# Optimization experiments

Measured on AMD Instinct MI355X. Metric: run time of the kernel, lower is better.

Reference implementation:

```python
import jax, jax.numpy as jnp
import numpy as np

B, S, D, H, E, K = 2, 1024, 1024, 4096, 8, 2
HE = 4 * D  # expert FFN inner dim
LN_EPS = 1e-5


def layernorm(x, g, b):
    m = x.mean(-1, keepdims=True)
    v = ((x - m) ** 2).mean(-1, keepdims=True)
    return (x - m) * jax.lax.rsqrt(v + LN_EPS) * g + b


def pos_encoding(S, D):
    pos = jnp.arange(S, dtype=jnp.float32)[:, None]
    i = jnp.arange(0, D, 2, dtype=jnp.float32)
    div = jnp.exp(-(jnp.log(10000.0)) * i / D)
    pe = jnp.zeros((S, D), dtype=jnp.float32)
    pe = pe.at[:, 0::2].set(jnp.sin(pos * div))
    pe = pe.at[:, 1::2].set(jnp.cos(pos * div))
    return pe


def setup_inputs() -> dict:
    key = jax.random.key(0)
    ks = jax.random.split(key, 16)
    w = lambda k, sh, s=0.02: (jax.random.normal(k, sh, dtype=jnp.float32) * s)
    return {
        "x": jax.random.normal(ks[0], (B, S, D), dtype=jnp.float32),
        # router: LayerNorm -> Linear(D,H) -> GELU -> Linear(H,E)
        "r_ln_g": jnp.ones((D,), jnp.float32), "r_ln_b": jnp.zeros((D,), jnp.float32),
        "r_w1": w(ks[1], (D, H)), "r_b1": jnp.zeros((H,), jnp.float32),
        "r_w2": w(ks[2], (H, E)), "r_b2": jnp.zeros((E,), jnp.float32),
        "temperature": jnp.ones((1,), jnp.float32) * 0.07,
        # stacked expert params: LayerNorm -> Linear(D,HE) -> GELU -> Linear(HE,D)
        "e_ln_g": jnp.ones((E, D), jnp.float32), "e_ln_b": jnp.zeros((E, D), jnp.float32),
        "e_w1": w(ks[3], (E, D, HE)), "e_b1": jnp.zeros((E, HE), jnp.float32),
        "e_w2": w(ks[4], (E, HE, D)), "e_b2": jnp.zeros((E, D), jnp.float32),
        # combiner: LayerNorm -> Linear(D,2D) -> GELU -> Linear(2D,D)
        "c_ln_g": jnp.ones((D,), jnp.float32), "c_ln_b": jnp.zeros((D,), jnp.float32),
        "c_w1": w(ks[5], (D, 2 * D)), "c_b1": jnp.zeros((2 * D,), jnp.float32),
        "c_w2": w(ks[6], (2 * D, D)), "c_b2": jnp.zeros((D,), jnp.float32),
        "o_ln_g": jnp.ones((D,), jnp.float32), "o_ln_b": jnp.zeros((D,), jnp.float32),
    }


def reference(x, r_ln_g, r_ln_b, r_w1, r_b1, r_w2, r_b2, temperature,
              e_ln_g, e_ln_b, e_w1, e_b1, e_w2, e_b2,
              c_ln_g, c_ln_b, c_w1, c_b1, c_w2, c_b2, o_ln_g, o_ln_b):
    gelu = lambda t: jax.nn.gelu(t, approximate=False)
    h = x + pos_encoding(S, D)[None]  # [B,S,D]
    # router logits with learned temperature
    r = layernorm(h, r_ln_g, r_ln_b)
    r = gelu(jnp.einsum("bsd,dh->bsh", r, r_w1) + r_b1)
    logits = (jnp.einsum("bsh,he->bse", r, r_w2) + r_b2) / temperature
    probs = jax.nn.softmax(logits, axis=-1)  # [B,S,E]
    topk_p, topk_i = jax.lax.top_k(probs, K)
    # sparse gate [B,S,E]: softmax prob on selected experts, 0 elsewhere
    gate = (jax.nn.one_hot(topk_i, E, dtype=probs.dtype) * topk_p[..., None]).sum(-2)
    # per-expert FFN on all tokens (dense reference of dispatch/compute/combine)
    m = h.mean(-1, keepdims=True)
    v = ((h - m) ** 2).mean(-1, keepdims=True)
    xhat = (h - m) * jax.lax.rsqrt(v + LN_EPS)  # [B,S,D], shared LN stats
    y = xhat[None] * e_ln_g[:, None, None, :] + e_ln_b[:, None, None, :]  # [E,B,S,D]
    f = gelu(jnp.einsum("ebsd,edh->ebsh", y, e_w1) + e_b1[:, None, None, :])
    f = jnp.einsum("ebsh,ehd->ebsd", f, e_w2) + e_b2[:, None, None, :]
    combined = jnp.einsum("bse,ebsd->bsd", gate, f)
    # expert combiner MLP + residual + output norm
    c = layernorm(combined, c_ln_g, c_ln_b)
    c = gelu(jnp.einsum("bsd,de->bse", c, c_w1) + c_b1)
    c = jnp.einsum("bse,ed->bsd", c, c_w2) + c_b2
    return layernorm(h + c, o_ln_g, o_ln_b)
```

## Files before the change

### kernel.cpp

```cpp
#include <hip/hip_runtime.h>
#include <stdint.h>

#define TOK 2048
#define DD  1024
#define RH  4096
#define HE  4096
#define NE  8
#define CH  2048
#define MAXTILE 40
#define MAXROWS 5120
#define KSC2 2

using bf16x8 = __attribute__((ext_vector_type(8))) short;
using f32x4  = __attribute__((ext_vector_type(4))) float;

__device__ __forceinline__ unsigned short f2bf(float f) {
  union { float f; uint32_t u; } v; v.f = f;
  uint32_t r = (v.u + 0x7fffu + ((v.u >> 16) & 1u)) >> 16;
  return (unsigned short)r;
}
__device__ __forceinline__ float bf2f(unsigned short h) {
  union { uint32_t u; float f; } v; v.u = ((uint32_t)h) << 16;
  return v.f;
}
__device__ __forceinline__ float gelu_f(float x) {
  return 0.5f * x * (1.0f + erff(x * 0.70710678118654752440f));
}

#define GLD(SRC, DST) __builtin_amdgcn_global_load_lds( \
    (const __attribute__((address_space(1))) uint32_t*)(const void*)(SRC), \
    (__attribute__((address_space(3))) uint32_t*)(void*)(DST), 16, 0, 0)

__device__ __forceinline__ void block_ln_stats(float s1, float s2, float& mean, float& rstd) {
  #pragma unroll
  for (int off = 32; off > 0; off >>= 1) {
    s1 += __shfl_down(s1, off);
    s2 += __shfl_down(s2, off);
  }
  __shared__ float sh[8];
  int tid = threadIdx.x;
  if ((tid & 63) == 0) { sh[tid >> 6] = s1; sh[4 + (tid >> 6)] = s2; }
  __syncthreads();
  float t1 = sh[0] + sh[1] + sh[2] + sh[3];
  float t2 = sh[4] + sh[5] + sh[6] + sh[7];
  mean = t1 * (1.0f / 1024.0f);
  float var = t2 * (1.0f / 1024.0f) - mean * mean;
  rstd = rsqrtf(var + 1e-5f);
}

__global__ void k_prep(const float* __restrict__ x, float* __restrict__ h,
                       float* __restrict__ xh32, unsigned short* __restrict__ xhi,
                       unsigned short* __restrict__ xlo, int* __restrict__ cnt,
                       int* __restrict__ fillc, int* __restrict__ nflag,
                       int* __restrict__ tok_of) {
  int t = blockIdx.x;
  int s = t & 1023;
  int tid = threadIdx.x;
  float4 xv = ((const float4*)(x + (size_t)t * DD))[tid];
  float v[4]; float s1 = 0.f, s2 = 0.f;
  #pragma unroll
  for (int kp = 0; kp < 2; ++kp) {
    float i2 = (float)(tid * 4 + kp * 2);
    float div = expf(-9.2103403719761836f * i2 * (1.0f / 1024.0f));
    float ang = (float)s * div;
    float sn, cs;
    sincosf(ang, &sn, &cs);
    float xe = (kp == 0) ? xv.x : xv.z;
    float xo = (kp == 0) ? xv.y : xv.w;
    v[kp * 2] = xe + sn; v[kp * 2 + 1] = xo + cs;
  }
  #pragma unroll
  for (int k = 0; k < 4; ++k) { s1 += v[k]; s2 += v[k] * v[k]; }
  float mean, rstd;
  block_ln_stats(s1, s2, mean, rstd);
  float4 ho; ho.x = v[0]; ho.y = v[1]; ho.z = v[2]; ho.w = v[3];
  ((float4*)(h + (size_t)t * DD))[tid] = ho;
  float xn[4]; unsigned short hh[4], ll[4];
  #pragma unroll
  for (int k = 0; k < 4; ++k) {
    xn[k] = (v[k] - mean) * rstd;
    hh[k] = f2bf(xn[k]);
    ll[k] = f2bf(xn[k] - bf2f(hh[k]));
  }
  float4 xo4; xo4.x = xn[0]; xo4.y = xn[1]; xo4.z = xn[2]; xo4.w = xn[3];
  ((float4*)(xh32 + (size_t)t * DD))[tid] = xo4;
  ushort4 h4; h4.x = hh[0]; h4.y = hh[1]; h4.z = hh[2]; h4.w = hh[3];
  ((ushort4*)(xhi + (size_t)t * DD))[tid] = h4;
  ushort4 l4; l4.x = ll[0]; l4.y = ll[1]; l4.z = ll[2]; l4.w = ll[3];
  ((ushort4*)(xlo + (size_t)t * DD))[tid] = l4;
  if (t == 0) {
    for (int i = tid; i < MAXROWS; i += 256) tok_of[i] = 0;
    if (tid < NE) { cnt[tid] = 0; fillc[tid] = 0; }
    if (tid == 0) nflag[0] = 0;
  }
}

__global__ void k_tconv(const float* __restrict__ in, const float* __restrict__ g,
                        unsigned short* __restrict__ out, int D, int N,
                        long long in_bs, long long g_bs, long long out_bs) {
  __shared__ float tile[64][65];
  int e = blockIdx.z;
  const float* inb = in + (size_t)e * in_bs;
  unsigned short* outb = out + (size_t)e * out_bs;
  int n0 = blockIdx.x * 64, d0 = blockIdx.y * 64;
  int c4 = threadIdx.x & 15;
  int r0 = threadIdx.x >> 4;
  #pragma unroll
  for (int rr = 0; rr < 4; ++rr) {
    int dl = r0 + rr * 16;
    float4 v = *(const float4*)(inb + (size_t)(d0 + dl) * N + n0 + c4 * 4);
    if (g) {
      float gv = g[(size_t)e * g_bs + d0 + dl];
      v.x *= gv; v.y *= gv; v.z *= gv; v.w *= gv;
    }
    tile[dl][c4 * 4 + 0] = v.x; tile[dl][c4 * 4 + 1] = v.y;
    tile[dl][c4 * 4 + 2] = v.z; tile[dl][c4 * 4 + 3] = v.w;
  }
  __syncthreads();
  int q = threadIdx.x & 15;
  int nb = threadIdx.x >> 4;
  #pragma unroll
  for (int rr = 0; rr < 4; ++rr) {
    int nl = nb + rr * 16;
    ushort4 o;
    o.x = f2bf(tile[q * 4 + 0][nl]); o.y = f2bf(tile[q * 4 + 1][nl]);
    o.z = f2bf(tile[q * 4 + 2][nl]); o.w = f2bf(tile[q * 4 + 3][nl]);
    *(ushort4*)(outb + (size_t)(n0 + nl) * D + d0 + q * 4) = o;
  }
}

__global__ void k_tconv_split(const float* __restrict__ in, const float* __restrict__ g,
                              unsigned short* __restrict__ oh, unsigned short* __restrict__ ol,
                              float* __restrict__ o32, int D, int N) {
  __shared__ float tile[32][33];
  int n0 = blockIdx.x * 32, d0 = blockIdx.y * 32;
  int tn = threadIdx.x & 31, tr = threadIdx.x >> 5;
  #pragma unroll
  for (int rr = 0; rr < 4; ++rr) {
    int dl = tr + rr * 8;
    float v = in[(size_t)(d0 + dl) * N + n0 + tn];
    if (g) v *= g[d0 + dl];
    tile[dl][tn] = v;
  }
  __syncthreads();
  #pragma unroll
  for (int rr = 0; rr < 4; ++rr) {
    int nl = tr + rr * 8;
    float v = tile[tn][nl];
    size_t off = (size_t)(n0 + nl) * D + d0 + tn;
    unsigned short hi = f2bf(v);
    oh[off] = hi;
    ol[off] = f2bf(v - bf2f(hi));
    o32[off] = v;
  }
}

__global__ void k_foldbias(const float* __restrict__ w, const float* __restrict__ lnb,
                           const float* __restrict__ b1, float* __restrict__ outb,
                           int D, int N, long long w_bs, long long lnb_bs,
                           long long b_bs, long long o_bs) {
  int e = blockIdx.y;
  int n = blockIdx.x * 256 + threadIdx.x;
  const float* wb = w + (size_t)e * w_bs;
  const float* lb = lnb + (size_t)e * lnb_bs;
  float acc = b1[(size_t)e * b_bs + n];
  for (int d = 0; d < D; ++d) {
    float l = lb[d];
    if (l != 0.f) acc += l * wb[(size_t)d * N + n];
  }
  outb[(size_t)e * o_bs + n] = acc;
}

template <int DO_GELU, int OUT_BF16>
__global__ __launch_bounds__(256)
void k_gemm_n64(const unsigned short* __restrict__ A, const unsigned short* __restrict__ B,
                const float* __restrict__ bias, void* __restrict__ Cv, int N, int K,
                int kslice, long long c_slice) {
  __shared__ __align__(16) unsigned short As[128 * 32];
  __shared__ __align__(16) unsigned short Bs[64 * 32];
  const int tid = threadIdx.x;
  const int w = tid >> 6, lane = tid & 63;
  const int q = lane >> 4, r16 = lane & 15;
  const int kz = blockIdx.z;
  const int n0 = blockIdx.x * 64, m0 = blockIdx.y * 128;
  f32x4 acc[4][2];
  #pragma unroll
  for (int i = 0; i < 4; ++i)
    #pragma unroll
    for (int j = 0; j < 2; ++j) acc[i][j] = (f32x4){0.f, 0.f, 0.f, 0.f};
  const int srow = w * 32 + (lane >> 2);
  const int bsrow = (w < 2) ? srow : 0;
  const int scol = (lane & 3) * 8;
  const unsigned short* a_src = A + (size_t)(m0 + srow) * K + scol + (size_t)kz * kslice;
  const unsigned short* b_src = B + (size_t)(n0 + bsrow) * K + scol + (size_t)kz * kslice;
  unsigned short* a_dst = &As[w * 1024];
  unsigned short* b_dst = &Bs[(w & 1) * 1024];
  const int wm = w >> 1, wn = w & 1;
  for (int kt = 0; kt < kslice; kt += 32) {
    GLD(a_src + kt, a_dst);
    GLD(a_src + kt + (size_t)16 * K, a_dst + 512);
    if (w < 2) {
      GLD(b_src + kt, b_dst);
      GLD(b_src + kt + (size_t)16 * K, b_dst + 512);
    }
    __syncthreads();
    bf16x8 af[4], bfv[2];
    #pragma unroll
    for (int i = 0; i < 4; ++i)
      af[i] = *(const bf16x8*)&As[(wm * 64 + i * 16 + r16) * 32 + q * 8];
    #pragma unroll
    for (int j = 0; j < 2; ++j)
      bfv[j] = *(const bf16x8*)&Bs[(wn * 32 + j * 16 + r16) * 32 + q * 8];
    #pragma unroll
    for (int i = 0; i < 4; ++i)
      #pragma unroll
      for (int j = 0; j < 2; ++j)
        acc[i][j] = __builtin_amdgcn_mfma_f32_16x16x32_bf16(af[i], bfv[j], acc[i][j], 0, 0, 0);
    __syncthreads();
  }
  #pragma unroll
  for (int j = 0; j < 2; ++j) {
    int col = n0 + wn * 32 + j * 16 + r16;
    float bv = bias ? bias[col] : 0.f;
    #pragma unroll
    for (int i = 0; i < 4; ++i) {
      int row = m0 + wm * 64 + i * 16 + q * 4;
      #pragma unroll
      for (int t2 = 0; t2 < 4; ++t2) {
        float vv = acc[i][j][t2] + bv;
        if (DO_GELU) vv = gelu_f(vv);
        if (OUT_BF16) ((unsigned short*)Cv)[(size_t)(row + t2) * N + col] = f2bf(vv);
        else ((float*)Cv)[(size_t)kz * c_slice + (size_t)(row + t2) * N + col] = vv;
      }
    }
  }
}

__global__ __launch_bounds__(256)
void k_gemm_g1(const unsigned short* __restrict__ A, const unsigned short* __restrict__ W,
               const float* __restrict__ bias, unsigned short* __restrict__ C,
               const int* __restrict__ tok_of, const int* __restrict__ tile_e,
               const int* __restrict__ tile_r0, const int* __restrict__ ntiles) {
  if ((int)blockIdx.y >= *ntiles) return;
  __shared__ __align__(16) unsigned short As[128 * 32];
  __shared__ __align__(16) unsigned short Bs[128 * 32];
  const int tid = threadIdx.x;
  const int w = tid >> 6, lane = tid & 63;
  const int q = lane >> 4, r16 = lane & 15;
  const int e = tile_e[blockIdx.y];
  const int row0 = tile_r0[blockIdx.y];
  const int n0 = blockIdx.x * 128;
  f32x4 acc[4][4];
  #pragma unroll
  for (int i = 0; i < 4; ++i)
    #pragma unroll
    for (int j = 0; j < 4; ++j) acc[i][j] = (f32x4){0.f, 0.f, 0.f, 0.f};
  const int srow = w * 32 + (lane >> 2);
  const int scol = (lane & 3) * 8;
  const int t0 = tok_of[row0 + srow];
  const int t1 = tok_of[row0 + srow + 16];
  const unsigned short* a_src0 = A + (size_t)t0 * DD + scol;
  const unsigned short* a_src1 = A + (size_t)t1 * DD + scol;
  const unsigned short* b_src = W + (size_t)e * RH * DD + (size_t)(n0 + srow) * DD + scol;
  unsigned short* a_dst = &As[w * 1024];
  unsigned short* b_dst = &Bs[w * 1024];
  const int wm = w >> 1, wn = w & 1;
  for (int kt = 0; kt < DD; kt += 32) {
    GLD(a_src0 + kt, a_dst);
    GLD(a_src1 + kt, a_dst + 512);
    GLD(b_src + kt, b_dst);
    GLD(b_src + kt + (size_t)16 * DD, b_dst + 512);
    __syncthreads();
    bf16x8 af[4], bfv[4];
    #pragma unroll
    for (int i = 0; i < 4; ++i)
      af[i] = *(const bf16x8*)&As[(wm * 64 + i * 16 + r16) * 32 + q * 8];
    #pragma unroll
    for (int j = 0; j < 4; ++j)
      bfv[j] = *(const bf16x8*)&Bs[(wn * 64 + j * 16 + r16) * 32 + q * 8];
    #pragma unroll
    for (int i = 0; i < 4; ++i)
      #pragma unroll
      for (int j = 0; j < 4; ++j)
        acc[i][j] = __builtin_amdgcn_mfma_f32_16x16x32_bf16(af[i], bfv[j], acc[i][j], 0, 0, 0);
    __syncthreads();
  }
  #pragma unroll
  for (int j = 0; j < 4; ++j) {
    int col = n0 + wn * 64 + j * 16 + r16;
    float bv = bias[(size_t)e * RH + col];
    #pragma unroll
    for (int i = 0; i < 4; ++i) {
      int row = row0 + wm * 64 + i * 16 + q * 4;
      #pragma unroll
      for (int t2 = 0; t2 < 4; ++t2)
        C[(size_t)(row + t2) * RH + col] = f2bf(gelu_f(acc[i][j][t2] + bv));
    }
  }
}

__global__ __launch_bounds__(256)
void k_gemm_g2n(const unsigned short* __restrict__ A, const unsigned short* __restrict__ W,
                unsigned short* __restrict__ C, const int* __restrict__ tile_e,
                const int* __restrict__ tile_r0, const int* __restrict__ ntiles) {
  if ((int)blockIdx.y >= *ntiles) return;
  __shared__ __align__(16) unsigned short As[128 * 32];
  __shared__ __align__(16) unsigned short Bs[64 * 32];
  const int tid = threadIdx.x;
  const int w = tid >> 6, lane = tid & 63;
  const int q = lane >> 4, r16 = lane & 15;
  const int e = tile_e[blockIdx.y];
  const int row0 = tile_r0[blockIdx.y];
  const int n0 = blockIdx.x * 64;
  f32x4 acc[4][2];
  #pragma unroll
  for (int i = 0; i < 4; ++i)
    #pragma unroll
    for (int j = 0; j < 2; ++j) acc[i][j] = (f32x4){0.f, 0.f, 0.f, 0.f};
  const int srow = w * 32 + (lane >> 2);
  const int bsrow = (w < 2) ? srow : 0;
  const int scol = (lane & 3) * 8;
  const unsigned short* a_src = A + (size_t)(row0 + srow) * HE + scol;
  const unsigned short* b_src = W + (size_t)e * DD * HE + (size_t)(n0 + bsrow) * HE + scol;
  unsigned short* a_dst = &As[w * 1024];
  unsigned short* b_dst = &Bs[(w & 1) * 1024];
  const int wm = w >> 1, wn = w & 1;
  for (int kt = 0; kt < HE; kt += 32) {
    GLD(a_src + kt, a_dst);
    GLD(a_src + kt + (size_t)16 * HE, a_dst + 512);
    if (w < 2) {
      GLD(b_src + kt, b_dst);
      GLD(b_src + kt + (size_t)16 * HE, b_dst + 512);
    }
    __syncthreads();
    bf16x8 af[4], bfv[2];
    #pragma unroll
    for (int i = 0; i < 4; ++i)
      af[i] = *(const bf16x8*)&As[(wm * 64 + i * 16 + r16) * 32 + q * 8];
    #pragma unroll
    for (int j = 0; j < 2; ++j)
      bfv[j] = *(const bf16x8*)&Bs[(wn * 32 + j * 16 + r16) * 32 + q * 8];
    #pragma unroll
    for (int i = 0; i < 4; ++i)
      #pragma unroll
      for (int j = 0; j < 2; ++j)
        acc[i][j] = __builtin_amdgcn_mfma_f32_16x16x32_bf16(af[i], bfv[j], acc[i][j], 0, 0, 0);
    __syncthreads();
  }
  #pragma unroll
  for (int j = 0; j < 2; ++j) {
    int col = n0 + wn * 32 + j * 16 + r16;
    #pragma unroll
    for (int i = 0; i < 4; ++i) {
      int row = row0 + wm * 64 + i * 16 + q * 4;
      #pragma unroll
      for (int t2 = 0; t2 < 4; ++t2)
        C[(size_t)(row + t2) * DD + col] = f2bf(acc[i][j][t2]);
    }
  }
}

__global__ __launch_bounds__(256)
void k_gemm_split(const unsigned short* __restrict__ Ah, const unsigned short* __restrict__ Al,
                  const unsigned short* __restrict__ Bh, const unsigned short* __restrict__ Bl,
                  const float* __restrict__ bias, const float* __restrict__ w2,
                  float* __restrict__ lgp, int K) {
  __shared__ __align__(16) unsigned short Ahs[128 * 32];
  __shared__ __align__(16) unsigned short Als[128 * 32];
  __shared__ __align__(16) unsigned short Bhs[128 * 32];
  __shared__ __align__(16) unsigned short Bls[128 * 32];
  const int tid = threadIdx.x;
  const int w = tid >> 6, lane = tid & 63;
  const int q = lane >> 4, r16 = lane & 15;
  const int n0 = blockIdx.x * 128, m0 = blockIdx.y * 128;
  f32x4 acc[4][4];
  #pragma unroll
  for (int i = 0; i < 4; ++i)
    #pragma unroll
    for (int j = 0; j < 4; ++j) acc[i][j] = (f32x4){0.f, 0.f, 0.f, 0.f};
  const int srow = w * 32 + (lane >> 2);
  const int scol = (lane & 3) * 8;
  const unsigned short* ah_src = Ah + (size_t)(m0 + srow) * K + scol;
  const unsigned short* al_src = Al + (size_t)(m0 + srow) * K + scol;
  const unsigned short* bh_src = Bh + (size_t)(n0 + srow) * K + scol;
  const unsigned short* bl_src = Bl + (size_t)(n0 + srow) * K + scol;
  const int wm = w >> 1, wn = w & 1;
  for (int kt = 0; kt < K; kt += 32) {
    GLD(ah_src + kt, &Ahs[w * 1024]);
    GLD(ah_src + kt + (size_t)16 * K, &Ahs[w * 1024 + 512]);
    GLD(al_src + kt, &Als[w * 1024]);
    GLD(al_src + kt + (size_t)16 * K, &Als[w * 1024 + 512]);
    GLD(bh_src + kt, &Bhs[w * 1024]);
    GLD(bh_src + kt + (size_t)16 * K, &Bhs[w * 1024 + 512]);
    GLD(bl_src + kt, &Bls[w * 1024]);
    GLD(bl_src + kt + (size_t)16 * K, &Bls[w * 1024 + 512]);
    __syncthreads();
    bf16x8 ah[4], al[4], bh[4], bl[4];
    #pragma unroll
    for (int i = 0; i < 4; ++i) {
      int o = (wm * 64 + i * 16 + r16) * 32 + q * 8;
      ah[i] = *(const bf16x8*)&Ahs[o];
      al[i] = *(const bf16x8*)&Als[o];
    }
    #pragma unroll
    for (int j = 0; j < 4; ++j) {
      int o = (wn * 64 + j * 16 + r16) * 32 + q * 8;
      bh[j] = *(const bf16x8*)&Bhs[o];
      bl[j] = *(const bf16x8*)&Bls[o];
    }
    #pragma unroll
    for (int i = 0; i < 4; ++i)
      #pragma unroll
      for (int j = 0; j < 4; ++j) {
        acc[i][j] = __builtin_amdgcn_mfma_f32_16x16x32_bf16(ah[i], bh[j], acc[i][j], 0, 0, 0);
        acc[i][j] = __builtin_amdgcn_mfma_f32_16x16x32_bf16(al[i], bh[j], acc[i][j], 0, 0, 0);
        acc[i][j] = __builtin_amdgcn_mfma_f32_16x16x32_bf16(ah[i], bl[j], acc[i][j], 0, 0, 0);
      }
    __syncthreads();
  }
  float w2v[4][8], bv[4];
  #pragma unroll
  for (int j = 0; j < 4; ++j) {
    int col = n0 + wn * 64 + j * 16 + r16;
    bv[j] = bias[col];
    const float4* wr = (const float4*)(w2 + (size_t)col * 8);
    float4 u = wr[0], v2 = wr[1];
    w2v[j][0] = u.x;  w2v[j][1] = u.y;  w2v[j][2] = u.z;  w2v[j][3] = u.w;
    w2v[j][4] = v2.x; w2v[j][5] = v2.y; w2v[j][6] = v2.z; w2v[j][7] = v2.w;
  }
  float* plog = (float*)Ahs;
  #pragma unroll
  for (int idx = 0; idx < 4; ++idx) plog[idx * 256 + tid] = 0.f;
  __syncthreads();
  #pragma unroll
  for (int i = 0; i < 4; ++i)
    #pragma unroll
    for (int t2 = 0; t2 < 4; ++t2) {
      int rloc = wm * 64 + i * 16 + q * 4 + t2;
      float a8[8];
      #pragma unroll
      for (int e2 = 0; e2 < 8; ++e2) a8[e2] = 0.f;
      #pragma unroll
      for (int j = 0; j < 4; ++j) {
        float v = gelu_f(acc[i][j][t2] + bv[j]);
        #pragma unroll
        for (int e2 = 0; e2 < 8; ++e2) a8[e2] += v * w2v[j][e2];
      }
      #pragma unroll
      for (int off = 8; off > 0; off >>= 1)
        #pragma unroll
        for (int e2 = 0; e2 < 8; ++e2) a8[e2] += __shfl_down(a8[e2], off, 16);
      if (r16 == 0) {
        #pragma unroll
        for (int e2 = 0; e2 < 8; ++e2) atomicAdd(&plog[rloc * 8 + e2], a8[e2]);
      }
    }
  __syncthreads();
  float4* dst = (float4*)(lgp + ((size_t)blockIdx.x * TOK + m0) * 8);
  dst[tid] = ((float4*)plog)[tid];
}

__global__ void k_gate1(const float* __restrict__ lgp, const float* __restrict__ b2,
                        const float* __restrict__ temp, int* __restrict__ sel_i,
                        float* __restrict__ sel_p, int* __restrict__ flag,
                        float* __restrict__ lg32, int* __restrict__ nflag,
                        int* __restrict__ ftok) {
  int t = blockIdx.x * 256 + threadIdx.x;
  if (t >= TOK) return;
  float s8[NE];
  #pragma unroll
  for (int e = 0; e < NE; ++e) s8[e] = 0.f;
  for (int c = 0; c < RH / 128; ++c) {
    const float4* p = (const float4*)(lgp + ((size_t)c * TOK + t) * 8);
    float4 u = p[0], v = p[1];
    s8[0] += u.x; s8[1] += u.y; s8[2] += u.z; s8[3] += u.w;
    s8[4] += v.x; s8[5] += v.y; s8[6] += v.z; s8[7] += v.w;
  }
  float tmp = temp[0];
  float lg[NE];
  #pragma unroll
  for (int e = 0; e < NE; ++e) lg[e] = (s8[e] + b2[e]) / tmp;
  float mx = lg[0];
  for (int e = 1; e < NE; ++e) mx = fmaxf(mx, lg[e]);
  float p[NE], se = 0.f;
  for (int e = 0; e < NE; ++e) { p[e] = expf(lg[e] - mx); se += p[e]; }
  float inv = 1.f / se;
  int i1 = 0; float p1 = p[0];
  for (int e = 1; e < NE; ++e) if (p[e] > p1) { p1 = p[e]; i1 = e; }
  int i2 = -1; float p2 = -1.f;
  for (int e = 0; e < NE; ++e) if (e != i1 && p[e] > p2) { p2 = p[e]; i2 = e; }
  sel_i[t * 2] = i1; sel_i[t * 2 + 1] = i2;
  sel_p[t * 2] = p1 * inv; sel_p[t * 2 + 1] = p2 * inv;
  float a1 = -1e30f, a2 = -1e30f, a3 = -1e30f;
  for (int e = 0; e < NE; ++e) {
    float vv = lg[e];
    if (vv > a1) { a3 = a2; a2 = a1; a1 = vv; }
    else if (vv > a2) { a3 = a2; a2 = vv; }
    else if (vv > a3) a3 = vv;
  }
  int fl = (a2 - a3 < 0.01f) ? 1 : 0;
  flag[t] = fl;
  if (fl) {
    int pidx = atomicAdd(nflag, 1);
    ftok[pidx] = t;
    #pragma unroll
    for (int e = 0; e < NE; ++e) lg32[(size_t)t * NE + e] = 0.f;
  }
}

__global__ void k_triage2(const int* __restrict__ nflag, const int* __restrict__ ftok,
                          const float* __restrict__ xh32, const float* __restrict__ W32,
                          const float* __restrict__ biasr, const float* __restrict__ w2,
                          float* __restrict__ lg32) {
  int nf = *nflag;
  __shared__ float xs[DD];
  __shared__ float sh2[4][NE];
  int tid = threadIdx.x;
  int w = tid >> 6, lane = tid & 63;
  for (int idx = blockIdx.y; idx < nf; idx += (int)gridDim.y) {
    int t = ftok[idx];
    ((float4*)xs)[tid] = ((const float4*)(xh32 + (size_t)t * DD))[tid];
    __syncthreads();
    int hh0 = blockIdx.x * 64 + w * 16;
    float acc[NE];
    #pragma unroll
    for (int e = 0; e < NE; ++e) acc[e] = 0.f;
    #pragma unroll
    for (int r = 0; r < 16; ++r) {
      int hh = hh0 + r;
      const float4* wrow = (const float4*)(W32 + (size_t)hh * DD);
      float s = 0.f;
      #pragma unroll
      for (int c = 0; c < 4; ++c) {
        float4 wv = wrow[lane + 64 * c];
        float4 xv = ((const float4*)xs)[lane + 64 * c];
        s += wv.x * xv.x + wv.y * xv.y + wv.z * xv.z + wv.w * xv.w;
      }
      #pragma unroll
      for (int off = 32; off > 0; off >>= 1) s += __shfl_down(s, off);
      if (lane == 0) {
        float r1 = gelu_f(s + biasr[hh]);
        const float* wr = w2 + (size_t)hh * NE;
        #pragma unroll
        for (int e = 0; e < NE; ++e) acc[e] += r1 * wr[e];
      }
    }
    if (lane == 0) {
      #pragma unroll
      for (int e = 0; e < NE; ++e) sh2[w][e] = acc[e];
    }
    __syncthreads();
    if (tid < NE) {
      float v = sh2[0][tid] + sh2[1][tid] + sh2[2][tid] + sh2[3][tid];
      atomicAdd(&lg32[(size_t)t * NE + tid], v);
    }
    __syncthreads();
  }
}

__global__ void k_gate2(const int* __restrict__ flag, const float* __restrict__ lg32,
                        const float* __restrict__ b2, const float* __restrict__ temp,
                        int* __restrict__ sel_i, float* __restrict__ sel_p,
                        int* __restrict__ cnt) {
  int t = blockIdx.x * 256 + threadIdx.x;
  if (t >= TOK) return;
  int i1, i2;
  if (flag[t]) {
    float tmp = temp[0];
    float lg[NE];
    #pragma unroll
    for (int e = 0; e < NE; ++e) lg[e] = (lg32[(size_t)t * NE + e] + b2[e]) / tmp;
    float mx = lg[0];
    for (int e = 1; e < NE; ++e) mx = fmaxf(mx, lg[e]);
    float p[NE], se = 0.f;
    for (int e = 0; e < NE; ++e) { p[e] = expf(lg[e] - mx); se += p[e]; }
    float inv = 1.f / se;
    i1 = 0; float p1 = p[0];
    for (int e = 1; e < NE; ++e) if (p[e] > p1) { p1 = p[e]; i1 = e; }
    i2 = -1; float p2 = -1.f;
    for (int e = 0; e < NE; ++e) if (e != i1 && p[e] > p2) { p2 = p[e]; i2 = e; }
    sel_i[t * 2] = i1; sel_i[t * 2 + 1] = i2;
    sel_p[t * 2] = p1 * inv; sel_p[t * 2 + 1] = p2 * inv;
  } else {
    i1 = sel_i[t * 2]; i2 = sel_i[t * 2 + 1];
  }
  atomicAdd(&cnt[i1], 1);
  atomicAdd(&cnt[i2], 1);
}

__global__ void k_offsets(const int* __restrict__ cnt, int* __restrict__ off,
                          int* __restrict__ tile_e, int* __restrict__ tile_r0,
                          int* __restrict__ ntiles) {
  if (threadIdx.x == 0) {
    int cur = 0, nt = 0;
    for (int e = 0; e < NE; ++e) {
      off[e] = cur;
      int n = (cnt[e] + 127) >> 7;
      for (int k = 0; k < n; ++k) { tile_e[nt] = e; tile_r0[nt] = cur + 128 * k; nt++; }
      cur += n * 128;
    }
    *ntiles = nt;
  }
}

__global__ void k_fill(const int* __restrict__ sel_i, const int* __restrict__ off,
                       int* __restrict__ fill, int* __restrict__ slotarr,
                       int* __restrict__ tok_of) {
  int t = blockIdx.x * 256 + threadIdx.x;
  if (t >= TOK) return;
  #pragma unroll
  for (int j = 0; j < 2; ++j) {
    int e = sel_i[2 * t + j];
    int pos = atomicAdd(&fill[e], 1);
    int s = off[e] + pos;
    slotarr[2 * t + j] = s;
    tok_of[s] = t;
  }
}

__global__ void k_combine2(const int* __restrict__ slotarr, const int* __restrict__ sel_i,
                           const float* __restrict__ sel_p, const unsigned short* __restrict__ pairout,
                           const float* __restrict__ e_b2, unsigned short* __restrict__ xc) {
  int t = blockIdx.x, tid = threadIdx.x;
  int s0 = slotarr[t * 2], s1 = slotarr[t * 2 + 1];
  int e0 = sel_i[t * 2], e1 = sel_i[t * 2 + 1];
  float w0 = sel_p[t * 2], w1 = sel_p[t * 2 + 1];
  ushort4 u0 = ((const ushort4*)(pairout + (size_t)s0 * DD))[tid];
  ushort4 u1 = ((const ushort4*)(pairout + (size_t)s1 * DD))[tid];
  float4 b0 = ((const float4*)(e_b2 + (size_t)e0 * DD))[tid];
  float4 b1v = ((const float4*)(e_b2 + (size_t)e1 * DD))[tid];
  float v[4];
  v[0] = w0 * (bf2f(u0.x) + b0.x) + w1 * (bf2f(u1.x) + b1v.x);
  v[1] = w0 * (bf2f(u0.y) + b0.y) + w1 * (bf2f(u1.y) + b1v.y);
  v[2] = w0 * (bf2f(u0.z) + b0.z) + w1 * (bf2f(u1.z) + b1v.z);
  v[3] = w0 * (bf2f(u0.w) + b0.w) + w1 * (bf2f(u1.w) + b1v.w);
  float s1f = v[0] + v[1] + v[2] + v[3];
  float s2f = v[0]*v[0] + v[1]*v[1] + v[2]*v[2] + v[3]*v[3];
  float mean, rstd;
  block_ln_stats(s1f, s2f, mean, rstd);
  ushort4 o;
  o.x = f2bf((v[0] - mean) * rstd); o.y = f2bf((v[1] - mean) * rstd);
  o.z = f2bf((v[2] - mean) * rstd); o.w = f2bf((v[3] - mean) * rstd);
  ((ushort4*)(xc + (size_t)t * DD))[tid] = o;
}

__global__ void k_final(const float* __restrict__ h, const float* __restrict__ c2p,
                        const float* __restrict__ cb2, const float* __restrict__ og,
                        const float* __restrict__ ob, float* __restrict__ out) {
  int t = blockIdx.x, tid = threadIdx.x;
  float4 hv = ((const float4*)(h + (size_t)t * DD))[tid];
  float ax = 0.f, ay = 0.f, az = 0.f, aw = 0.f;
  #pragma unroll
  for (int z = 0; z < KSC2; ++z) {
    float4 u = ((const float4*)(c2p + (size_t)z * TOK * DD + (size_t)t * DD))[tid];
    ax += u.x; ay += u.y; az += u.z; aw += u.w;
  }
  float4 cb = ((const float4*)cb2)[tid];
  float v[4] = {hv.x + ax + cb.x, hv.y + ay + cb.y, hv.z + az + cb.z, hv.w + aw + cb.w};
  float s1 = v[0] + v[1] + v[2] + v[3];
  float s2 = v[0]*v[0] + v[1]*v[1] + v[2]*v[2] + v[3]*v[3];
  float mean, rstd;
  block_ln_stats(s1, s2, mean, rstd);
  float4 gv = ((const float4*)og)[tid];
  float4 bv = ((const float4*)ob)[tid];
  float4 o;
  o.x = (v[0] - mean) * rstd * gv.x + bv.x;
  o.y = (v[1] - mean) * rstd * gv.y + bv.y;
  o.z = (v[2] - mean) * rstd * gv.z + bv.z;
  o.w = (v[3] - mean) * rstd * gv.w + bv.w;
  ((float4*)(out + (size_t)t * DD))[tid] = o;
}

extern "C" void kernel_launch(void* const* d_in, const int* in_sizes, int n_in,
                              void* d_out, int out_size, void* d_ws, size_t ws_size,
                              hipStream_t stream) {
  (void)in_sizes; (void)n_in; (void)out_size; (void)ws_size;
  const float* x      = (const float*)d_in[0];
  const float* r_ln_g = (const float*)d_in[1];
  const float* r_ln_b = (const float*)d_in[2];
  const float* r_w1   = (const float*)d_in[3];
  const float* r_b1   = (const float*)d_in[4];
  const float* r_w2   = (const float*)d_in[5];
  const float* r_b2   = (const float*)d_in[6];
  const float* temp   = (const float*)d_in[7];
  const float* e_ln_g = (const float*)d_in[8];
  const float* e_ln_b = (const float*)d_in[9];
  const float* e_w1   = (const float*)d_in[10];
  const float* e_b1   = (const float*)d_in[11];
  const float* e_w2   = (const float*)d_in[12];
  const float* e_b2   = (const float*)d_in[13];
  const float* c_ln_g = (const float*)d_in[14];
  const float* c_ln_b = (const float*)d_in[15];
  const float* c_w1   = (const float*)d_in[16];
  const float* c_b1   = (const float*)d_in[17];
  const float* c_w2   = (const float*)d_in[18];
  const float* c_b2   = (const float*)d_in[19];
  const float* o_ln_g = (const float*)d_in[20];
  const float* o_ln_b = (const float*)d_in[21];
  float* out = (float*)d_out;

  char* base = (char*)d_ws;
  long long cur = 0;
  auto take = [&](long long sz) { char* r = base + cur; cur += (sz + 255) & ~255LL; return r; };

  float* h      = (float*)take(8388608);
  float* xh32   = (float*)take(8388608);
  unsigned short* xhi = (unsigned short*)take(4194304);
  unsigned short* xlo = (unsigned short*)take(4194304);
  unsigned short* WrH = (unsigned short*)take(8388608);
  unsigned short* WrL = (unsigned short*)take(8388608);
  float* Wr32   = (float*)take(16777216);
  float* biasr  = (float*)take(16384);
  float* lgp    = (float*)take((long long)(RH/128) * TOK * NE * 4);
  int*   flag   = (int*)take(8192);
  float* lg32   = (float*)take(65536);
  int*   sel_i  = (int*)take(16384);
  float* sel_p  = (float*)take(16384);
  int*   cnt    = (int*)take(256);
  int*   off    = (int*)take(256);
  int*   fillc  = (int*)take(256);
  int*   tile_e = (int*)take(256);
  int*   tile_r0= (int*)take(256);
  int*   ntiles = (int*)take(256);
  int*   nflag  = (int*)take(256);
  int*   ftok   = (int*)take(TOK * 4);
  int*   slotarr= (int*)take(16384);
  int*   tok_of = (int*)take(MAXROWS * 4);
  unsigned short* We1 = (unsigned short*)take(67108864);
  float* be1    = (float*)take(131072);
  unsigned short* We2 = (unsigned short*)take(67108864);
  unsigned short* Wc1 = (unsigned short*)take(4194304);
  float* bc1    = (float*)take(8192);
  unsigned short* Wc2 = (unsigned short*)take(4194304);
  unsigned short* xc  = (unsigned short*)take(4194304);
  unsigned short* c1  = (unsigned short*)take(8388608);
  unsigned short* F1g = (unsigned short*)take((long long)MAXROWS * RH * 2);
  unsigned short* pairout = (unsigned short*)take((long long)MAXROWS * DD * 2);
  float* c2part = (float*)take((long long)KSC2 * TOK * DD * 4);

  k_prep<<<TOK, 256, 0, stream>>>(x, h, xh32, xhi, xlo, cnt, fillc, nflag, tok_of);
  k_tconv_split<<<dim3(RH/32, DD/32, 1), 256, 0, stream>>>(r_w1, r_ln_g, WrH, WrL, Wr32, DD, RH);
  k_tconv<<<dim3(RH/64, DD/64, NE), 256, 0, stream>>>(e_w1, e_ln_g, We1, DD, RH,
      (long long)DD*RH, (long long)DD, (long long)RH*DD);
  k_tconv<<<dim3(DD/64, HE/64, NE), 256, 0, stream>>>(e_w2, nullptr, We2, HE, DD,
      (long long)HE*DD, 0LL, (long long)DD*HE);
  k_tconv<<<dim3(CH/64, DD/64, 1), 256, 0, stream>>>(c_w1, c_ln_g, Wc1, DD, CH, 0LL, 0LL, 0LL);
  k_tconv<<<dim3(DD/64, CH/64, 1), 256, 0, stream>>>(c_w2, nullptr, Wc2, CH, DD, 0LL, 0LL, 0LL);
  k_foldbias<<<dim3(RH/256, 1), 256, 0, stream>>>(r_w1, r_ln_b, r_b1, biasr, DD, RH, 0LL, 0LL, 0LL, 0LL);
  k_foldbias<<<dim3(RH/256, NE), 256, 0, stream>>>(e_w1, e_ln_b, e_b1, be1, DD, RH,
      (long long)DD*RH, (long long)DD, (long long)RH, (long long)RH);
  k_foldbias<<<dim3(CH/256, 1), 256, 0, stream>>>(c_w1, c_ln_b, c_b1, bc1, DD, CH, 0LL, 0LL, 0LL, 0LL);

  k_gemm_split<<<dim3(RH/128, TOK/128, 1), 256, 0, stream>>>(xhi, xlo, WrH, WrL, biasr,
      r_w2, lgp, DD);
  k_gate1<<<TOK/256, 256, 0, stream>>>(lgp, r_b2, temp, sel_i, sel_p, flag, lg32, nflag, ftok);
  k_triage2<<<dim3(RH/64, 32), 256, 0, stream>>>(nflag, ftok, xh32, Wr32, biasr, r_w2, lg32);
  k_gate2<<<TOK/256, 256, 0, stream>>>(flag, lg32, r_b2, temp, sel_i, sel_p, cnt);

  k_offsets<<<1, 64, 0, stream>>>(cnt, off, tile_e, tile_r0, ntiles);
  k_fill<<<TOK/256, 256, 0, stream>>>(sel_i, off, fillc, slotarr, tok_of);

  k_gemm_g1<<<dim3(RH/128, MAXTILE), 256, 0, stream>>>(xhi, We1, be1, F1g,
      tok_of, tile_e, tile_r0, ntiles);
  k_gemm_g2n<<<dim3(DD/64, MAXTILE), 256, 0, stream>>>(F1g, We2, pairout,
      tile_e, tile_r0, ntiles);

  k_combine2<<<TOK, 256, 0, stream>>>(slotarr, sel_i, sel_p, pairout, e_b2, xc);
  k_gemm_n64<1,1><<<dim3(CH/64, TOK/128, 1), 256, 0, stream>>>(xc, Wc1, bc1, (void*)c1,
      CH, DD, DD, 0LL);
  k_gemm_n64<0,0><<<dim3(DD/64, TOK/128, KSC2), 256, 0, stream>>>(c1, Wc2, nullptr,
      (void*)c2part, DD, CH, CH/KSC2, (long long)TOK * DD);
  k_final<<<TOK, 256, 0, stream>>>(h, c2part, c_b2, o_ln_g, o_ln_b, out);
}
```

Before: 1.050 ms.

## Split-K expert down-projection with fp32 partials, drop router weight low-part

The expert second GEMM now uses 128x128 tiles with a 4-way split along K and writes fp32 partial sums, which the combine kernel adds up. This replaces 64-wide tiles with one long K loop. The router GEMM drops the low-order bf16 part of the weights, cutting one of three MFMAs per step and one of four operand streams. The near-tie threshold for exact fp32 re-evaluation is widened to make up for the lost precision. The trade is more fp32 partial traffic and more tokens sent to the fp32 triage path.

```diff
diff --git a/kernel.cpp b/kernel.cpp
--- a/kernel.cpp
+++ b/kernel.cpp
@@ -9,6 +9,7 @@
 #define CH  2048
 #define MAXTILE 40
 #define MAXROWS 5120
+#define KSG2 4
 #define KSC2 2
 
 using bf16x8 = __attribute__((ext_vector_type(8))) short;
@@ -130,8 +131,8 @@
 }
 
 __global__ void k_tconv_split(const float* __restrict__ in, const float* __restrict__ g,
-                              unsigned short* __restrict__ oh, unsigned short* __restrict__ ol,
-                              float* __restrict__ o32, int D, int N) {
+                              unsigned short* __restrict__ oh, float* __restrict__ o32,
+                              int D, int N) {
   __shared__ float tile[32][33];
   int n0 = blockIdx.x * 32, d0 = blockIdx.y * 32;
   int tn = threadIdx.x & 31, tr = threadIdx.x >> 5;
@@ -148,9 +149,7 @@
     int nl = tr + rr * 8;
     float v = tile[tn][nl];
     size_t off = (size_t)(n0 + nl) * D + d0 + tn;
-    unsigned short hi = f2bf(v);
-    oh[off] = hi;
-    ol[off] = f2bf(v - bf2f(hi));
+    oh[off] = f2bf(v);
     o32[off] = v;
   }
 }
@@ -300,75 +299,72 @@
 }
 
 __global__ __launch_bounds__(256)
-void k_gemm_g2n(const unsigned short* __restrict__ A, const unsigned short* __restrict__ W,
-                unsigned short* __restrict__ C, const int* __restrict__ tile_e,
-                const int* __restrict__ tile_r0, const int* __restrict__ ntiles) {
+void k_gemm_g2(const unsigned short* __restrict__ A, const unsigned short* __restrict__ W,
+               float* __restrict__ C, const int* __restrict__ tile_e,
+               const int* __restrict__ tile_r0, const int* __restrict__ ntiles) {
   if ((int)blockIdx.y >= *ntiles) return;
   __shared__ __align__(16) unsigned short As[128 * 32];
-  __shared__ __align__(16) unsigned short Bs[64 * 32];
+  __shared__ __align__(16) unsigned short Bs[128 * 32];
   const int tid = threadIdx.x;
   const int w = tid >> 6, lane = tid & 63;
   const int q = lane >> 4, r16 = lane & 15;
   const int e = tile_e[blockIdx.y];
   const int row0 = tile_r0[blockIdx.y];
-  const int n0 = blockIdx.x * 64;
-  f32x4 acc[4][2];
+  const int n0 = blockIdx.x * 128;
+  const int kz = blockIdx.z;
+  f32x4 acc[4][4];
   #pragma unroll
   for (int i = 0; i < 4; ++i)
     #pragma unroll
-    for (int j = 0; j < 2; ++j) acc[i][j] = (f32x4){0.f, 0.f, 0.f, 0.f};
+    for (int j = 0; j < 4; ++j) acc[i][j] = (f32x4){0.f, 0.f, 0.f, 0.f};
   const int srow = w * 32 + (lane >> 2);
-  const int bsrow = (w < 2) ? srow : 0;
   const int scol = (lane & 3) * 8;
-  const unsigned short* a_src = A + (size_t)(row0 + srow) * HE + scol;
-  const unsigned short* b_src = W + (size_t)e * DD * HE + (size_t)(n0 + bsrow) * HE + scol;
+  const unsigned short* a_src = A + (size_t)(row0 + srow) * HE + scol + (size_t)kz * (HE / KSG2);
+  const unsigned short* b_src = W + (size_t)e * DD * HE + (size_t)(n0 + srow) * HE + scol
+                                + (size_t)kz * (HE / KSG2);
   unsigned short* a_dst = &As[w * 1024];
-  unsigned short* b_dst = &Bs[(w & 1) * 1024];
+  unsigned short* b_dst = &Bs[w * 1024];
   const int wm = w >> 1, wn = w & 1;
-  for (int kt = 0; kt < HE; kt += 32) {
+  for (int kt = 0; kt < HE / KSG2; kt += 32) {
     GLD(a_src + kt, a_dst);
     GLD(a_src + kt + (size_t)16 * HE, a_dst + 512);
-    if (w < 2) {
-      GLD(b_src + kt, b_dst);
-      GLD(b_src + kt + (size_t)16 * HE, b_dst + 512);
-    }
-    __syncthreads();
-    bf16x8 af[4], bfv[2];
+    GLD(b_src + kt, b_dst);
+    GLD(b_src + kt + (size_t)16 * HE, b_dst + 512);
+    __syncthreads();
+    bf16x8 af[4], bfv[4];
     #pragma unroll
     for (int i = 0; i < 4; ++i)
       af[i] = *(const bf16x8*)&As[(wm * 64 + i * 16 + r16) * 32 + q * 8];
     #pragma unroll
-    for (int j = 0; j < 2; ++j)
-      bfv[j] = *(const bf16x8*)&Bs[(wn * 32 + j * 16 + r16) * 32 + q * 8];
+    for (int j = 0; j < 4; ++j)
+      bfv[j] = *(const bf16x8*)&Bs[(wn * 64 + j * 16 + r16) * 32 + q * 8];
     #pragma unroll
     for (int i = 0; i < 4; ++i)
       #pragma unroll
-      for (int j = 0; j < 2; ++j)
+      for (int j = 0; j < 4; ++j)
         acc[i][j] = __builtin_amdgcn_mfma_f32_16x16x32_bf16(af[i], bfv[j], acc[i][j], 0, 0, 0);
     __syncthreads();
   }
   #pragma unroll
-  for (int j = 0; j < 2; ++j) {
-    int col = n0 + wn * 32 + j * 16 + r16;
+  for (int j = 0; j < 4; ++j) {
+    int col = n0 + wn * 64 + j * 16 + r16;
     #pragma unroll
     for (int i = 0; i < 4; ++i) {
       int row = row0 + wm * 64 + i * 16 + q * 4;
       #pragma unroll
       for (int t2 = 0; t2 < 4; ++t2)
-        C[(size_t)(row + t2) * DD + col] = f2bf(acc[i][j][t2]);
+        C[(size_t)kz * MAXROWS * DD + (size_t)(row + t2) * DD + col] = acc[i][j][t2];
     }
   }
 }
 
 __global__ __launch_bounds__(256)
 void k_gemm_split(const unsigned short* __restrict__ Ah, const unsigned short* __restrict__ Al,
-                  const unsigned short* __restrict__ Bh, const unsigned short* __restrict__ Bl,
-                  const float* __restrict__ bias, const float* __restrict__ w2,
-                  float* __restrict__ lgp, int K) {
+                  const unsigned short* __restrict__ Bh, const float* __restrict__ bias,
+                  const float* __restrict__ w2, float* __restrict__ lgp, int K) {
   __shared__ __align__(16) unsigned short Ahs[128 * 32];
   __shared__ __align__(16) unsigned short Als[128 * 32];
   __shared__ __align__(16) unsigned short Bhs[128 * 32];
-  __shared__ __align__(16) unsigned short Bls[128 * 32];
   const int tid = threadIdx.x;
   const int w = tid >> 6, lane = tid & 63;
   const int q = lane >> 4, r16 = lane & 15;
@@ -383,7 +379,6 @@
   const unsigned short* ah_src = Ah + (size_t)(m0 + srow) * K + scol;
   const unsigned short* al_src = Al + (size_t)(m0 + srow) * K + scol;
   const unsigned short* bh_src = Bh + (size_t)(n0 + srow) * K + scol;
-  const unsigned short* bl_src = Bl + (size_t)(n0 + srow) * K + scol;
   const int wm = w >> 1, wn = w & 1;
   for (int kt = 0; kt < K; kt += 32) {
     GLD(ah_src + kt, &Ahs[w * 1024]);
@@ -392,10 +387,8 @@
     GLD(al_src + kt + (size_t)16 * K, &Als[w * 1024 + 512]);
     GLD(bh_src + kt, &Bhs[w * 1024]);
     GLD(bh_src + kt + (size_t)16 * K, &Bhs[w * 1024 + 512]);
-    GLD(bl_src + kt, &Bls[w * 1024]);
-    GLD(bl_src + kt + (size_t)16 * K, &Bls[w * 1024 + 512]);
-    __syncthreads();
-    bf16x8 ah[4], al[4], bh[4], bl[4];
+    __syncthreads();
+    bf16x8 ah[4], al[4], bh[4];
     #pragma unroll
     for (int i = 0; i < 4; ++i) {
       int o = (wm * 64 + i * 16 + r16) * 32 + q * 8;
@@ -406,7 +399,6 @@
     for (int j = 0; j < 4; ++j) {
       int o = (wn * 64 + j * 16 + r16) * 32 + q * 8;
       bh[j] = *(const bf16x8*)&Bhs[o];
-      bl[j] = *(const bf16x8*)&Bls[o];
     }
     #pragma unroll
     for (int i = 0; i < 4; ++i)
@@ -414,7 +406,6 @@
       for (int j = 0; j < 4; ++j) {
         acc[i][j] = __builtin_amdgcn_mfma_f32_16x16x32_bf16(ah[i], bh[j], acc[i][j], 0, 0, 0);
         acc[i][j] = __builtin_amdgcn_mfma_f32_16x16x32_bf16(al[i], bh[j], acc[i][j], 0, 0, 0);
-        acc[i][j] = __builtin_amdgcn_mfma_f32_16x16x32_bf16(ah[i], bl[j], acc[i][j], 0, 0, 0);
       }
     __syncthreads();
   }
@@ -498,7 +489,7 @@
     else if (vv > a2) { a3 = a2; a2 = vv; }
     else if (vv > a3) a3 = vv;
   }
-  int fl = (a2 - a3 < 0.01f) ? 1 : 0;
+  int fl = (a2 - a3 < 0.08f) ? 1 : 0;
   flag[t] = fl;
   if (fl) {
     int pidx = atomicAdd(nflag, 1);
@@ -619,21 +610,28 @@
 }
 
 __global__ void k_combine2(const int* __restrict__ slotarr, const int* __restrict__ sel_i,
-                           const float* __restrict__ sel_p, const unsigned short* __restrict__ pairout,
+                           const float* __restrict__ sel_p, const float* __restrict__ pairpart,
                            const float* __restrict__ e_b2, unsigned short* __restrict__ xc) {
   int t = blockIdx.x, tid = threadIdx.x;
   int s0 = slotarr[t * 2], s1 = slotarr[t * 2 + 1];
   int e0 = sel_i[t * 2], e1 = sel_i[t * 2 + 1];
   float w0 = sel_p[t * 2], w1 = sel_p[t * 2 + 1];
-  ushort4 u0 = ((const ushort4*)(pairout + (size_t)s0 * DD))[tid];
-  ushort4 u1 = ((const ushort4*)(pairout + (size_t)s1 * DD))[tid];
+  float a0x = 0.f, a0y = 0.f, a0z = 0.f, a0w = 0.f;
+  float a1x = 0.f, a1y = 0.f, a1z = 0.f, a1w = 0.f;
+  #pragma unroll
+  for (int z = 0; z < KSG2; ++z) {
+    float4 u = ((const float4*)(pairpart + (size_t)z * MAXROWS * DD + (size_t)s0 * DD))[tid];
+    a0x += u.x; a0y += u.y; a0z += u.z; a0w += u.w;
+    float4 v = ((const float4*)(pairpart + (size_t)z * MAXROWS * DD + (size_t)s1 * DD))[tid];
+    a1x += v.x; a1y += v.y; a1z += v.z; a1w += v.w;
+  }
   float4 b0 = ((const float4*)(e_b2 + (size_t)e0 * DD))[tid];
   float4 b1v = ((const float4*)(e_b2 + (size_t)e1 * DD))[tid];
   float v[4];
-  v[0] = w0 * (bf2f(u0.x) + b0.x) + w1 * (bf2f(u1.x) + b1v.x);
-  v[1] = w0 * (bf2f(u0.y) + b0.y) + w1 * (bf2f(u1.y) + b1v.y);
-  v[2] = w0 * (bf2f(u0.z) + b0.z) + w1 * (bf2f(u1.z) + b1v.z);
-  v[3] = w0 * (bf2f(u0.w) + b0.w) + w1 * (bf2f(u1.w) + b1v.w);
+  v[0] = w0 * (a0x + b0.x) + w1 * (a1x + b1v.x);
+  v[1] = w0 * (a0y + b0.y) + w1 * (a1y + b1v.y);
+  v[2] = w0 * (a0z + b0.z) + w1 * (a1z + b1v.z);
+  v[3] = w0 * (a0w + b0.w) + w1 * (a1w + b1v.w);
   float s1f = v[0] + v[1] + v[2] + v[3];
   float s2f = v[0]*v[0] + v[1]*v[1] + v[2]*v[2] + v[3]*v[3];
   float mean, rstd;
@@ -708,7 +706,6 @@
   unsigned short* xhi = (unsigned short*)take(4194304);
   unsigned short* xlo = (unsigned short*)take(4194304);
   unsigned short* WrH = (unsigned short*)take(8388608);
-  unsigned short* WrL = (unsigned short*)take(8388608);
   float* Wr32   = (float*)take(16777216);
   float* biasr  = (float*)take(16384);
   float* lgp    = (float*)take((long long)(RH/128) * TOK * NE * 4);
@@ -735,11 +732,11 @@
   unsigned short* xc  = (unsigned short*)take(4194304);
   unsigned short* c1  = (unsigned short*)take(8388608);
   unsigned short* F1g = (unsigned short*)take((long long)MAXROWS * RH * 2);
-  unsigned short* pairout = (unsigned short*)take((long long)MAXROWS * DD * 2);
+  float* pairpart = (float*)take((long long)KSG2 * MAXROWS * DD * 4);
   float* c2part = (float*)take((long long)KSC2 * TOK * DD * 4);
 
   k_prep<<<TOK, 256, 0, stream>>>(x, h, xh32, xhi, xlo, cnt, fillc, nflag, tok_of);
-  k_tconv_split<<<dim3(RH/32, DD/32, 1), 256, 0, stream>>>(r_w1, r_ln_g, WrH, WrL, Wr32, DD, RH);
+  k_tconv_split<<<dim3(RH/32, DD/32, 1), 256, 0, stream>>>(r_w1, r_ln_g, WrH, Wr32, DD, RH);
   k_tconv<<<dim3(RH/64, DD/64, NE), 256, 0, stream>>>(e_w1, e_ln_g, We1, DD, RH,
       (long long)DD*RH, (long long)DD, (long long)RH*DD);
   k_tconv<<<dim3(DD/64, HE/64, NE), 256, 0, stream>>>(e_w2, nullptr, We2, HE, DD,
@@ -751,7 +748,7 @@
       (long long)DD*RH, (long long)DD, (long long)RH, (long long)RH);
   k_foldbias<<<dim3(CH/256, 1), 256, 0, stream>>>(c_w1, c_ln_b, c_b1, bc1, DD, CH, 0LL, 0LL, 0LL, 0LL);
 
-  k_gemm_split<<<dim3(RH/128, TOK/128, 1), 256, 0, stream>>>(xhi, xlo, WrH, WrL, biasr,
+  k_gemm_split<<<dim3(RH/128, TOK/128, 1), 256, 0, stream>>>(xhi, xlo, WrH, biasr,
       r_w2, lgp, DD);
   k_gate1<<<TOK/256, 256, 0, stream>>>(lgp, r_b2, temp, sel_i, sel_p, flag, lg32, nflag, ftok);
   k_triage2<<<dim3(RH/64, 32), 256, 0, stream>>>(nflag, ftok, xh32, Wr32, biasr, r_w2, lg32);
@@ -762,10 +759,10 @@
 
   k_gemm_g1<<<dim3(RH/128, MAXTILE), 256, 0, stream>>>(xhi, We1, be1, F1g,
       tok_of, tile_e, tile_r0, ntiles);
-  k_gemm_g2n<<<dim3(DD/64, MAXTILE), 256, 0, stream>>>(F1g, We2, pairout,
+  k_gemm_g2<<<dim3(DD/128, MAXTILE, KSG2), 256, 0, stream>>>(F1g, We2, pairpart,
       tile_e, tile_r0, ntiles);
 
-  k_combine2<<<TOK, 256, 0, stream>>>(slotarr, sel_i, sel_p, pairout, e_b2, xc);
+  k_combine2<<<TOK, 256, 0, stream>>>(slotarr, sel_i, sel_p, pairpart, e_b2, xc);
   k_gemm_n64<1,1><<<dim3(CH/64, TOK/128, 1), 256, 0, stream>>>(xc, Wc1, bc1, (void*)c1,
       CH, DD, DD, 0LL);
   k_gemm_n64<0,0><<<dim3(DD/64, TOK/128, KSC2), 256, 0, stream>>>(c1, Wc2, nullptr,
```

New measurement: 1.362 ms. +29.7%, slower.
